# Optimization experiments

Hardware: AMD Instinct MI355X
Metric: run time of the kernel (lower is better)

## Reference

```python
import jax, jax.numpy as jnp
import numpy as np

N = 50000          # nodes
E = 1_600_000      # edges
H = 64             # agg_hidden (heads=1, concat)
IN = 7             # in_channels
EDIM = 4           # edge_dim
G = 256            # num graphs in batch
FC = 128           # fc_hidden
NC = 2             # num_classes
SLOPE = 0.2        # GATv2 LeakyReLU negative slope


def setup_inputs() -> dict:
    key = jax.random.key(0)
    ks = jax.random.split(key, 24)
    s = 0.1
    d = {
        "x": jax.random.normal(ks[0], (N, IN), dtype=jnp.float32),
        "edge_index": jax.random.randint(ks[1], (2, E), 0, N, dtype=jnp.int32),
        "edge_attr": jax.random.normal(ks[2], (E, EDIM), dtype=jnp.float32),
        "batch": jnp.sort(jax.random.randint(ks[3], (N,), 0, G, dtype=jnp.int32)),
        # GATv2 layer 0 (in=7 -> 64)
        "Wl0": jax.random.normal(ks[4], (IN, H)) * s,
        "bl0": jnp.zeros((H,), jnp.float32),
        "Wr0": jax.random.normal(ks[5], (IN, H)) * s,
        "br0": jnp.zeros((H,), jnp.float32),
        "We0": jax.random.normal(ks[6], (EDIM, H)) * s,
        "att0": jax.random.normal(ks[7], (H,)) * s,
        "bias0": jnp.zeros((H,), jnp.float32),
        # GATv2 layer 1 (64 -> 64)
        "Wl1": jax.random.normal(ks[8], (H, H)) * s,
        "bl1": jnp.zeros((H,), jnp.float32),
        "Wr1": jax.random.normal(ks[9], (H, H)) * s,
        "br1": jnp.zeros((H,), jnp.float32),
        "We1": jax.random.normal(ks[10], (EDIM, H)) * s,
        "att1": jax.random.normal(ks[11], (H,)) * s,
        "bias1": jnp.zeros((H,), jnp.float32),
        # MLP head
        "fc1_w": jax.random.normal(ks[12], (H, FC)) * s,
        "fc1_b": jnp.zeros((FC,), jnp.float32),
        "fc2_w": jax.random.normal(ks[13], (FC, NC)) * s,
        "fc2_b": jnp.zeros((NC,), jnp.float32),
    }
    return d


def _gatv2(x, src, dst, edge_attr, Wl, bl, Wr, br, We, att, bias):
    # GATv2Conv (heads=1, concat=True, edge_dim=EDIM), eval mode (no dropout)
    xl = x @ Wl + bl                         # source-side projection [N,H]
    xr = x @ Wr + br                         # target-side projection [N,H]
    e = xl[src] + xr[dst] + edge_attr @ We   # per-edge pre-activation [E,H]
    score = jax.nn.leaky_relu(e, SLOPE) @ att  # [E]
    # segment softmax over destination nodes
    m = jax.ops.segment_max(score, dst, num_segments=N)
    ex = jnp.exp(score - m[dst])
    den = jax.ops.segment_sum(ex, dst, num_segments=N)
    alpha = ex / (den[dst] + 1e-16)
    out = jax.ops.segment_sum(xl[src] * alpha[:, None], dst, num_segments=N)
    return out + bias


def reference(x, edge_index, edge_attr, batch,
              Wl0, bl0, Wr0, br0, We0, att0, bias0,
              Wl1, bl1, Wr1, br1, We1, att1, bias1,
              fc1_w, fc1_b, fc2_w, fc2_b):
    src, dst = edge_index[0], edge_index[1]
    h = jax.nn.elu(_gatv2(x, src, dst, edge_attr, Wl0, bl0, Wr0, br0, We0, att0, bias0))
    h = jax.nn.elu(_gatv2(h, src, dst, edge_attr, Wl1, bl1, Wr1, br1, We1, att1, bias1))
    # global mean pool over graphs
    sums = jax.ops.segment_sum(h, batch, num_segments=G)
    cnt = jax.ops.segment_sum(jnp.ones((h.shape[0],), h.dtype), batch, num_segments=G)
    g = sums / jnp.maximum(cnt, 1.0)[:, None]      # [G,H]
    g = jax.nn.relu(g @ fc1_w + fc1_b)
    logits = g @ fc2_w + fc2_b
    return jax.nn.log_softmax(logits, axis=1)
```

## Files before the change

### kernel.cpp

```cpp
#include <hip/hip_runtime.h>
#include <hip/hip_fp16.h>

#define N_NODES 50000
#define N_EDGES 1600000
#define H 64
#define IN_CH 7
#define EDIM 4
#define G_GRAPHS 256
#define FC 128
#define NC 2
#define SLOPE 0.2f
#define NBUCK 196
#define EPB1 8192
#define NB1 ((N_EDGES + EPB1 - 1) / EPB1)
#define PAIR_BLOCKS ((N_NODES * 32 + 255) / 256)

typedef _Float16 h2v __attribute__((ext_vector_type(2)));

__device__ __forceinline__ float fdot2f(h2v a, h2v b, float c) {
#if defined(__has_builtin) && __has_builtin(__builtin_amdgcn_fdot2)
    return __builtin_amdgcn_fdot2(a, b, c, false);
#else
    return c + (float)a[0] * (float)b[0] + (float)a[1] * (float)b[1];
#endif
}

__device__ __forceinline__ float wave_sum_to63(float x) {
    x += __int_as_float(__builtin_amdgcn_update_dpp(0, __float_as_int(x), 0x111, 0xf, 0xf, true));
    x += __int_as_float(__builtin_amdgcn_update_dpp(0, __float_as_int(x), 0x112, 0xf, 0xf, true));
    x += __int_as_float(__builtin_amdgcn_update_dpp(0, __float_as_int(x), 0x114, 0xf, 0xf, true));
    x += __int_as_float(__builtin_amdgcn_update_dpp(0, __float_as_int(x), 0x118, 0xf, 0xf, true));
    x += __int_as_float(__builtin_amdgcn_update_dpp(0, __float_as_int(x), 0x142, 0xf, 0xf, true));
    x += __int_as_float(__builtin_amdgcn_update_dpp(0, __float_as_int(x), 0x143, 0xf, 0xf, true));
    return x;
}
__device__ __forceinline__ float lane63_bcast(float x) {
    return __int_as_float(__builtin_amdgcn_readlane(__float_as_int(x), 63));
}
__device__ __forceinline__ float readlane_f(float x, int i) {
    return __int_as_float(__builtin_amdgcn_readlane(__float_as_int(x), i));
}

__device__ __forceinline__ float gat_score(int4 ent,
        const __half2* __restrict__ xlh, const __half2* __restrict__ xrh,
        const __half2* __restrict__ weh, const __half2* __restrict__ atth) {
    __half2 ea01 = *reinterpret_cast<__half2*>(&ent.y);
    __half2 ea23 = *reinterpret_cast<__half2*>(&ent.z);
    __half2 e0 = __half2half2(__low2half(ea01));
    __half2 e1 = __half2half2(__high2half(ea01));
    __half2 e2 = __half2half2(__low2half(ea23));
    __half2 e3 = __half2half2(__high2half(ea23));
    const h2v sl = { (_Float16)SLOPE, (_Float16)SLOPE };
    const int4* xa = (const int4*)(xlh + (size_t)ent.x * 32);
    const int4* xb = (const int4*)(xrh + (size_t)ent.w * 32);
    float acc0 = 0.f, acc1 = 0.f;
#pragma unroll
    for (int k = 0; k < 8; ++k) {
        int4 va = xa[k];
        int4 vb = xb[k];
        const __half2* ha = reinterpret_cast<const __half2*>(&va);
        const __half2* hc = reinterpret_cast<const __half2*>(&vb);
#pragma unroll
        for (int j = 0; j < 4; ++j) {
            int c = k * 4 + j;
            __half2 v2 = __hadd2(ha[j], hc[j]);
            v2 = __hfma2(e0, weh[c * 4 + 0], v2);
            v2 = __hfma2(e1, weh[c * 4 + 1], v2);
            v2 = __hfma2(e2, weh[c * 4 + 2], v2);
            v2 = __hfma2(e3, weh[c * 4 + 3], v2);
            h2v vv = *reinterpret_cast<h2v*>(&v2);
            h2v Lv = __builtin_elementwise_max(vv, sl * vv);
            __half2 av = atth[c];
            if (j & 1)
                acc1 = fdot2f(Lv, *reinterpret_cast<h2v*>(&av), acc1);
            else
                acc0 = fdot2f(Lv, *reinterpret_cast<h2v*>(&av), acc0);
        }
    }
    return acc0 + acc1;
}

__global__ __launch_bounds__(256) void front_kernel(
        const int* __restrict__ dst, int* __restrict__ rank1, int* __restrict__ bhist,
        const float* __restrict__ xin,
        const float* __restrict__ Wl0, const float* __restrict__ bl0,
        const float* __restrict__ Wr0, const float* __restrict__ br0,
        __half2* __restrict__ xlh, __half2* __restrict__ xrh,
        const float* __restrict__ We0, const float* __restrict__ We1,
        const float* __restrict__ Wl1, const float* __restrict__ bl1,
        const float* __restrict__ Wr1, const float* __restrict__ br1,
        __half2* __restrict__ weh0, __half2* __restrict__ weh1,
        __half2* __restrict__ wt, float* __restrict__ bb,
        const float* __restrict__ att0, const float* __restrict__ att1,
        __half2* __restrict__ atth0, __half2* __restrict__ atth1) {
    __shared__ int hist[NBUCK];
    int b = blockIdx.x;
    int t = threadIdx.x;
    if (b < NB1) {
        if (t < NBUCK) hist[t] = 0;
        __syncthreads();
#pragma unroll
        for (int i = 0; i < EPB1 / 256; ++i) {
            int e = b * EPB1 + i * 256 + t;
            if (e < N_EDGES) {
                int k = dst[e] >> 8;
                rank1[e] = atomicAdd(&hist[k], 1);
            }
        }
        __syncthreads();
        if (t < NBUCK) bhist[b * NBUCK + t] = hist[t];
    } else if (b < NB1 + PAIR_BLOCKS) {
        int idx = (b - NB1) * 256 + t;
        if (idx < N_NODES * 32) {
            int n = idx >> 5;
            int c = idx & 31;
            const float* xi = xin + n * IN_CH;
            float2 bl2 = ((const float2*)bl0)[c];
            float2 br2 = ((const float2*)br0)[c];
            float al0 = bl2.x, al1 = bl2.y, ar0 = br2.x, ar1 = br2.y;
#pragma unroll
            for (int k = 0; k < IN_CH; ++k) {
                float xv = xi[k];
                float2 wl2 = ((const float2*)(Wl0 + k * H))[c];
                float2 wr2 = ((const float2*)(Wr0 + k * H))[c];
                al0 += xv * wl2.x; al1 += xv * wl2.y;
                ar0 += xv * wr2.x; ar1 += xv * wr2.y;
            }
            xlh[idx] = __floats2half2_rn(al0, al1);
            xrh[idx] = __floats2half2_rn(ar0, ar1);
        }
    } else {
        if (t < 32) {
            for (int k = 0; k < 4; ++k)
                weh0[t * 4 + k] = __floats2half2_rn(We0[k * H + 2 * t], We0[k * H + 2 * t + 1]);
        } else if (t < 64) {
            int c = t - 32;
            for (int k = 0; k < 4; ++k)
                weh1[c * 4 + k] = __floats2half2_rn(We1[k * H + 2 * c], We1[k * H + 2 * c + 1]);
        }
        if (t < 128) {
            const float* W = (t < 64) ? Wl1 : Wr1;
            int c = t & 63;
            for (int kk = 0; kk < 32; ++kk)
                wt[t * 32 + kk] = __floats2half2_rn(W[(2 * kk) * H + c], W[(2 * kk + 1) * H + c]);
            bb[t] = (t < 64) ? bl1[c] : br1[c];
        } else if (t < 160) {
            int c = t - 128;
            atth0[c] = __floats2half2_rn(att0[2 * c], att0[2 * c + 1]);
            atth1[c] = __floats2half2_rn(att1[2 * c], att1[2 * c + 1]);
        }
    }
}

__global__ __launch_bounds__(256) void bucket_scan_kernel(
        const int* __restrict__ bhist, int* __restrict__ bases, int* __restrict__ cb_start) {
    __shared__ int lds[256];
    int t = threadIdx.x;
    int run = 0;
    if (t < NBUCK) {
        for (int b = 0; b < NB1; ++b) {
            bases[b * NBUCK + t] = run;
            run += bhist[b * NBUCK + t];
        }
    }
    lds[t] = (t < NBUCK) ? run : 0;
    __syncthreads();
    for (int off = 1; off < 256; off <<= 1) {
        int x = (t >= off) ? lds[t - off] : 0;
        __syncthreads();
        lds[t] += x;
        __syncthreads();
    }
    if (t < NBUCK) cb_start[t] = lds[t] - run;
    if (t == NBUCK - 1) cb_start[NBUCK] = lds[t];
}

__global__ void coarse_scatter_kernel(const int* __restrict__ src, const int* __restrict__ dst,
                                      const int* __restrict__ rank1, const int* __restrict__ bases,
                                      const int* __restrict__ cb_start,
                                      const float* __restrict__ edge_attr,
                                      int4* __restrict__ tmp) {
    int e = blockIdx.x * blockDim.x + threadIdx.x;
    if (e >= N_EDGES) return;
    int d = dst[e];
    int k = d >> 8;
    int b = e / EPB1;
    int slot = cb_start[k] + bases[b * NBUCK + k] + rank1[e];
    float4 ea = ((const float4*)edge_attr)[e];
    __half2 h01 = __floats2half2_rn(ea.x, ea.y);
    __half2 h23 = __floats2half2_rn(ea.z, ea.w);
    int4 ent;
    ent.x = src[e];
    ent.y = *reinterpret_cast<int*>(&h01);
    ent.z = *reinterpret_cast<int*>(&h23);
    ent.w = d;
    tmp[slot] = ent;
}

__global__ __launch_bounds__(1024) void fine_sort_kernel(
        const int* __restrict__ cb_start, const int4* __restrict__ tmp,
        const __half2* __restrict__ xlh, const __half2* __restrict__ xrh,
        const __half2* __restrict__ weh, const __half2* __restrict__ atth,
        int4* __restrict__ csr, int* __restrict__ srcs,
        int* __restrict__ row_start, float* __restrict__ escore) {
    __shared__ int hist2[256];
    __shared__ int cursor[256];
    __shared__ int lds[256];
    int k = blockIdx.x;
    int t = threadIdx.x;
    int beg = cb_start[k], end = cb_start[k + 1];
    if (t < 256) hist2[t] = 0;
    __syncthreads();
    for (int i = beg + t; i < end; i += 1024)
        atomicAdd(&hist2[tmp[i].w & 255], 1);
    __syncthreads();
    int v = (t < 256) ? hist2[t] : 0;
    if (t < 256) lds[t] = v;
    __syncthreads();
    for (int off = 1; off < 256; off <<= 1) {
        int x = 0;
        if (t < 256 && t >= off) x = lds[t - off];
        __syncthreads();
        if (t < 256) lds[t] += x;
        __syncthreads();
    }
    if (t < 256) {
        int pre = lds[t] - v;
        cursor[t] = pre;
        int node = k * 256 + t;
        if (node <= N_NODES) row_start[node] = beg + pre;
    }
    __syncthreads();
    for (int i = beg + t; i < end; i += 1024) {
        int4 ent = tmp[i];
        int slot = beg + atomicAdd(&cursor[ent.w & 255], 1);
        csr[slot] = ent;
        srcs[slot] = ent.x;
        escore[slot] = gat_score(ent, xlh, xrh, weh, atth);
    }
}

__global__ __launch_bounds__(256) void proj1_kernel(
        const float* __restrict__ xin,
        const __half2* __restrict__ wt,
        const float* __restrict__ bb,
        __half2* __restrict__ xlh, __half2* __restrict__ xrh) {
    int g = __builtin_amdgcn_readfirstlane((int)(threadIdx.x >> 6));
    int lane = threadIdx.x & 63;
    int node = blockIdx.x * 64 + lane;
    if (node >= N_NODES) return;

    h2v xrow[32];
    const float4* xp = (const float4*)(xin + node * 64);
#pragma unroll
    for (int q = 0; q < 16; ++q) {
        float4 v = xp[q];
        __half2 a = __floats2half2_rn(v.x, v.y);
        __half2 b = __floats2half2_rn(v.z, v.w);
        xrow[2 * q]     = *reinterpret_cast<h2v*>(&a);
        xrow[2 * q + 1] = *reinterpret_cast<h2v*>(&b);
    }

    __half2* outp = (g < 2) ? xlh : xrh;
    int chbase = g * 32;
    int localbase = (g & 1) * 16;

#pragma unroll
    for (int cp = 0; cp < 16; ++cp) {
        int ch0 = chbase + 2 * cp;
        const h2v* w0 = (const h2v*)(wt + ch0 * 32);
        const h2v* w1 = (const h2v*)(wt + (ch0 + 1) * 32);
        float a0 = bb[ch0], a1 = bb[ch0 + 1];
#pragma unroll
        for (int kk = 0; kk < 32; ++kk) {
            a0 = fdot2f(xrow[kk], w0[kk], a0);
            a1 = fdot2f(xrow[kk], w1[kk], a1);
        }
        outp[node * 32 + localbase + cp] = __floats2half2_rn(a0, a1);
    }
}

__global__ __launch_bounds__(256) void score_kernel(
        const int4* __restrict__ csr,
        const __half2* __restrict__ xlh, const __half2* __restrict__ xrh,
        const __half2* __restrict__ weh, const __half2* __restrict__ atth,
        float* __restrict__ score) {
    int e = blockIdx.x * 256 + threadIdx.x;
    score[e] = gat_score(csr[e], xlh, xrh, weh, atth);
}

__global__ __launch_bounds__(256) void agg_kernel(
        const int* __restrict__ row_start,
        const int* __restrict__ srcs,
        const float* __restrict__ score,
        const __half2* __restrict__ xlh,
        const float* __restrict__ bias,
        float* __restrict__ out) {
    int wave = (blockIdx.x * blockDim.x + threadIdx.x) >> 6;
    if (wave >= N_NODES) return;
    int lane = threadIdx.x & 63;
    int c = lane & 31;
    int hb = lane >> 5;
    int d = wave;
    int beg = __builtin_amdgcn_readfirstlane(row_start[d]);
    int end = __builtin_amdgcn_readfirstlane(row_start[d + 1]);

    float l_lane = 0.f;
    float ax0 = 0.f, ay0 = 0.f, ax1 = 0.f, ay1 = 0.f;

    for (int cbeg = beg; cbeg < end; cbeg += 64) {
        int n = end - cbeg;
        float sc = score[cbeg + lane];
        float p = __expf(sc);
        p = (lane < n) ? p : 0.f;
        l_lane += p;

        int nn = min(n, 64);
        int j = 0;
        for (; j + 4 <= nn; j += 4) {
            int sA0 = __builtin_amdgcn_readfirstlane(srcs[cbeg + j + 0]);
            int sB0 = __builtin_amdgcn_readfirstlane(srcs[cbeg + j + 1]);
            int sA1 = __builtin_amdgcn_readfirstlane(srcs[cbeg + j + 2]);
            int sB1 = __builtin_amdgcn_readfirstlane(srcs[cbeg + j + 3]);
            float pA0 = readlane_f(p, j + 0), pB0 = readlane_f(p, j + 1);
            float pA1 = readlane_f(p, j + 2), pB1 = readlane_f(p, j + 3);
            int s0 = hb ? sB0 : sA0;
            int s1 = hb ? sB1 : sA1;
            float pv0 = hb ? pB0 : pA0;
            float pv1 = hb ? pB1 : pA1;
            float2 x0 = __half22float2(xlh[s0 * 32 + c]);
            float2 x1 = __half22float2(xlh[s1 * 32 + c]);
            ax0 += pv0 * x0.x; ay0 += pv0 * x0.y;
            ax1 += pv1 * x1.x; ay1 += pv1 * x1.y;
        }
        for (; j + 2 <= nn; j += 2) {
            int sA = __builtin_amdgcn_readfirstlane(srcs[cbeg + j + 0]);
            int sB = __builtin_amdgcn_readfirstlane(srcs[cbeg + j + 1]);
            float pA = readlane_f(p, j + 0), pB = readlane_f(p, j + 1);
            int s = hb ? sB : sA;
            float pv = hb ? pB : pA;
            float2 xf = __half22float2(xlh[s * 32 + c]);
            ax0 += pv * xf.x; ay0 += pv * xf.y;
        }
        if (j < nn) {
            int sA = __builtin_amdgcn_readfirstlane(srcs[cbeg + j]);
            float pA = readlane_f(p, j);
            float pv = hb ? 0.f : pA;
            float2 xf = __half22float2(xlh[sA * 32 + c]);
            ax0 += pv * xf.x; ay0 += pv * xf.y;
        }
    }

    float l = lane63_bcast(wave_sum_to63(l_lane));
    float accx = ax0 + ax1, accy = ay0 + ay1;
    accx += __shfl_xor(accx, 32, 64);
    accy += __shfl_xor(accy, 32, 64);
    if (hb == 0) {
        float inv = 1.f / (l + 1e-16f);
        float2 b2 = ((const float2*)bias)[c];
        float o0 = accx * inv + b2.x;
        float o1 = accy * inv + b2.y;
        o0 = o0 > 0.f ? o0 : expm1f(o0);
        o1 = o1 > 0.f ? o1 : expm1f(o1);
        ((float2*)out)[d * 32 + c] = float2{o0, o1};
    }
}

__global__ __launch_bounds__(256) void pool_head_kernel(
        const float* __restrict__ h, const int* __restrict__ batch,
        const float* __restrict__ fc1w, const float* __restrict__ fc1b,
        const float* __restrict__ fc2w, const float* __restrict__ fc2b,
        float* __restrict__ out) {
    int g = blockIdx.x;
    int lo = 0, hi = N_NODES;
    while (lo < hi) { int mid = (lo + hi) >> 1; if (batch[mid] < g) lo = mid + 1; else hi = mid; }
    int start = lo;
    hi = N_NODES;
    while (lo < hi) { int mid = (lo + hi) >> 1; if (batch[mid] < g + 1) lo = mid + 1; else hi = mid; }
    int end = lo;

    int lane = threadIdx.x & 63;
    int w = threadIdx.x >> 6;
    float s = 0.f;
    for (int n = start + w; n < end; n += 4) s += h[n * H + lane];
    __shared__ float red[4][H];
    __shared__ float gv[H];
    __shared__ float f[FC];
    __shared__ float lg[NC];
    red[w][lane] = s;
    __syncthreads();
    if (w == 0) {
        float tot = red[0][lane] + red[1][lane] + red[2][lane] + red[3][lane];
        gv[lane] = tot / fmaxf((float)(end - start), 1.f);
    }
    __syncthreads();
    int t = threadIdx.x;
    if (t < FC) {
        float acc = fc1b[t];
#pragma unroll 16
        for (int k = 0; k < H; ++k) acc += gv[k] * fc1w[k * FC + t];
        f[t] = fmaxf(acc, 0.f);
    }
    __syncthreads();
    if (t < NC) {
        float a = fc2b[t];
        for (int k = 0; k < FC; ++k) a += f[k] * fc2w[k * NC + t];
        lg[t] = a;
    }
    __syncthreads();
    if (t < NC) {
        float mx = fmaxf(lg[0], lg[1]);
        float lse = mx + logf(expf(lg[0] - mx) + expf(lg[1] - mx));
        out[g * NC + t] = lg[t] - lse;
    }
}

extern "C" void kernel_launch(void* const* d_in, const int* in_sizes, int n_in,
                              void* d_out, int out_size, void* d_ws, size_t ws_size,
                              hipStream_t stream) {
    const float* x         = (const float*)d_in[0];
    const int*   edge_idx  = (const int*)d_in[1];
    const float* edge_attr = (const float*)d_in[2];
    const int*   batch     = (const int*)d_in[3];
    const float* Wl0  = (const float*)d_in[4];
    const float* bl0  = (const float*)d_in[5];
    const float* Wr0  = (const float*)d_in[6];
    const float* br0  = (const float*)d_in[7];
    const float* We0  = (const float*)d_in[8];
    const float* att0 = (const float*)d_in[9];
    const float* bias0= (const float*)d_in[10];
    const float* Wl1  = (const float*)d_in[11];
    const float* bl1  = (const float*)d_in[12];
    const float* Wr1  = (const float*)d_in[13];
    const float* br1  = (const float*)d_in[14];
    const float* We1  = (const float*)d_in[15];
    const float* att1 = (const float*)d_in[16];
    const float* bias1= (const float*)d_in[17];
    const float* fc1w = (const float*)d_in[18];
    const float* fc1b = (const float*)d_in[19];
    const float* fc2w = (const float*)d_in[20];
    const float* fc2b = (const float*)d_in[21];

    __half2* xlh    = (__half2*)d_ws;
    __half2* xrh    = xlh + N_NODES * 32;
    float* C        = (float*)(xrh + N_NODES * 32);
    int4*  tmp      = (int4*)C;
    int4*  csr      = (int4*)(tmp + N_EDGES);
    int*   srcs     = (int*)(csr + N_EDGES);
    int*   row_start= srcs + N_EDGES;
    int*   rank1    = row_start + N_NODES + 1;
    float* escore   = (float*)rank1;
    int*   bhist    = rank1 + N_EDGES;
    int*   bases    = bhist + NB1 * NBUCK;
    int*   cb_start = bases + NB1 * NBUCK;
    __half2* weh0   = (__half2*)(cb_start + NBUCK + 1);
    __half2* weh1   = weh0 + 128;
    __half2* wt1    = weh1 + 128;
    float* bb1      = (float*)(wt1 + 128 * 32);
    __half2* atth0  = (__half2*)(bb1 + 128);
    __half2* atth1  = atth0 + 32;

    const int* src = edge_idx;
    const int* dst = edge_idx + N_EDGES;

    const int edgeBlocks = (N_EDGES + 255) / 256;
    const int waveBlocks = (N_NODES * 64 + 255) / 256;
    const int p1Blocks   = (N_NODES + 63) / 64;
    const int frontBlocks = NB1 + PAIR_BLOCKS + 1;

    front_kernel<<<frontBlocks, 256, 0, stream>>>(dst, rank1, bhist,
                                                  x, Wl0, bl0, Wr0, br0, xlh, xrh,
                                                  We0, We1, Wl1, bl1, Wr1, br1,
                                                  weh0, weh1, wt1, bb1,
                                                  att0, att1, atth0, atth1);
    bucket_scan_kernel<<<1, 256, 0, stream>>>(bhist, bases, cb_start);
    coarse_scatter_kernel<<<edgeBlocks, 256, 0, stream>>>(src, dst, rank1, bases, cb_start,
                                                          edge_attr, tmp);
    fine_sort_kernel<<<NBUCK, 1024, 0, stream>>>(cb_start, tmp, xlh, xrh, weh0, atth0,
                                                 csr, srcs, row_start, escore);

    agg_kernel<<<waveBlocks, 256, 0, stream>>>(row_start, srcs, escore, xlh, bias0, C);

    proj1_kernel<<<p1Blocks, 256, 0, stream>>>(C, wt1, bb1, xlh, xrh);
    score_kernel<<<edgeBlocks, 256, 0, stream>>>(csr, xlh, xrh, weh1, atth1, escore);
    agg_kernel<<<waveBlocks, 256, 0, stream>>>(row_start, srcs, escore, xlh, bias1, C);

    pool_head_kernel<<<G_GRAPHS, 256, 0, stream>>>(C, batch, fc1w, fc1b, fc2w, fc2b, (float*)d_out);
}
```

Measured before the change: 444.6 us.

## Replace two-level bucket sort with global atomic counting sort into CSR

Replaces the coarse-bucket histogram, bucket scan, coarse scatter and per-bucket fine sort with a single pass of global atomics on per-node counts. A one-block node scan then builds row_start, and one scatter writes the CSR entries straight into their final slots. Layer-0 scores move out of the fine sort into a separate score_kernel launch. This drops the intermediate tmp buffer pass and the block-local sorting, but brings contended global atomics on 50k counters, a serial single-block scan, and nondeterministic edge order within each row.

```diff
diff --git a/kernel.cpp b/kernel.cpp
--- a/kernel.cpp
+++ b/kernel.cpp
@@ -10,7 +10,6 @@
 #define FC 128
 #define NC 2
 #define SLOPE 0.2f
-#define NBUCK 196
 #define EPB1 8192
 #define NB1 ((N_EDGES + EPB1 - 1) / EPB1)
 #define PAIR_BLOCKS ((N_NODES * 32 + 255) / 256)
@@ -81,7 +80,7 @@
 }
 
 __global__ __launch_bounds__(256) void front_kernel(
-        const int* __restrict__ dst, int* __restrict__ rank1, int* __restrict__ bhist,
+        const int* __restrict__ dst, int* __restrict__ rank1, int* __restrict__ cnt,
         const float* __restrict__ xin,
         const float* __restrict__ Wl0, const float* __restrict__ bl0,
         const float* __restrict__ Wr0, const float* __restrict__ br0,
@@ -93,22 +92,15 @@
         __half2* __restrict__ wt, float* __restrict__ bb,
         const float* __restrict__ att0, const float* __restrict__ att1,
         __half2* __restrict__ atth0, __half2* __restrict__ atth1) {
-    __shared__ int hist[NBUCK];
     int b = blockIdx.x;
     int t = threadIdx.x;
     if (b < NB1) {
-        if (t < NBUCK) hist[t] = 0;
-        __syncthreads();
 #pragma unroll
         for (int i = 0; i < EPB1 / 256; ++i) {
             int e = b * EPB1 + i * 256 + t;
-            if (e < N_EDGES) {
-                int k = dst[e] >> 8;
-                rank1[e] = atomicAdd(&hist[k], 1);
-            }
-        }
-        __syncthreads();
-        if (t < NBUCK) bhist[b * NBUCK + t] = hist[t];
+            if (e < N_EDGES)
+                rank1[e] = atomicAdd(&cnt[dst[e]], 1);
+        }
     } else if (b < NB1 + PAIR_BLOCKS) {
         int idx = (b - NB1) * 256 + t;
         if (idx < N_NODES * 32) {
@@ -152,40 +144,43 @@
     }
 }
 
-__global__ __launch_bounds__(256) void bucket_scan_kernel(
-        const int* __restrict__ bhist, int* __restrict__ bases, int* __restrict__ cb_start) {
-    __shared__ int lds[256];
-    int t = threadIdx.x;
-    int run = 0;
-    if (t < NBUCK) {
-        for (int b = 0; b < NB1; ++b) {
-            bases[b * NBUCK + t] = run;
-            run += bhist[b * NBUCK + t];
-        }
-    }
-    lds[t] = (t < NBUCK) ? run : 0;
-    __syncthreads();
-    for (int off = 1; off < 256; off <<= 1) {
-        int x = (t >= off) ? lds[t - off] : 0;
-        __syncthreads();
-        lds[t] += x;
-        __syncthreads();
-    }
-    if (t < NBUCK) cb_start[t] = lds[t] - run;
-    if (t == NBUCK - 1) cb_start[NBUCK] = lds[t];
-}
-
-__global__ void coarse_scatter_kernel(const int* __restrict__ src, const int* __restrict__ dst,
-                                      const int* __restrict__ rank1, const int* __restrict__ bases,
-                                      const int* __restrict__ cb_start,
-                                      const float* __restrict__ edge_attr,
-                                      int4* __restrict__ tmp) {
-    int e = blockIdx.x * blockDim.x + threadIdx.x;
-    if (e >= N_EDGES) return;
+__global__ __launch_bounds__(1024) void node_scan_kernel(
+        const int* __restrict__ cnt, int* __restrict__ row_start) {
+    __shared__ int wsum[16];
+    __shared__ int tot;
+    int t = threadIdx.x, lane = t & 63, w = t >> 6;
+    const int CHUNK = (N_NODES + 1023) / 1024;
+    int b0 = min(t * CHUNK, N_NODES);
+    int b1 = min(b0 + CHUNK, N_NODES);
+    int s = 0;
+    for (int i = b0; i < b1; ++i) s += cnt[i];
+    int sc = s;
+#pragma unroll
+    for (int off = 1; off < 64; off <<= 1) {
+        int x = __shfl_up(sc, off, 64);
+        if (lane >= off) sc += x;
+    }
+    if (lane == 63) wsum[w] = sc;
+    __syncthreads();
+    if (t == 0) {
+        int run = 0;
+        for (int j = 0; j < 16; ++j) { int v = wsum[j]; wsum[j] = run; run += v; }
+        tot = run;
+    }
+    __syncthreads();
+    int run = wsum[w] + sc - s;
+    for (int i = b0; i < b1; ++i) { int v = cnt[i]; row_start[i] = run; run += v; }
+    if (t == 0) row_start[N_NODES] = tot;
+}
+
+__global__ void scatter_kernel(const int* __restrict__ src, const int* __restrict__ dst,
+                               const int* __restrict__ rank1,
+                               const int* __restrict__ row_start,
+                               const float* __restrict__ edge_attr,
+                               int4* __restrict__ csr, int* __restrict__ srcs) {
+    int e = blockIdx.x * 256 + threadIdx.x;
     int d = dst[e];
-    int k = d >> 8;
-    int b = e / EPB1;
-    int slot = cb_start[k] + bases[b * NBUCK + k] + rank1[e];
+    int slot = row_start[d] + rank1[e];
     float4 ea = ((const float4*)edge_attr)[e];
     __half2 h01 = __floats2half2_rn(ea.x, ea.y);
     __half2 h23 = __floats2half2_rn(ea.z, ea.w);
@@ -194,50 +189,8 @@
     ent.y = *reinterpret_cast<int*>(&h01);
     ent.z = *reinterpret_cast<int*>(&h23);
     ent.w = d;
-    tmp[slot] = ent;
-}
-
-__global__ __launch_bounds__(1024) void fine_sort_kernel(
-        const int* __restrict__ cb_start, const int4* __restrict__ tmp,
-        const __half2* __restrict__ xlh, const __half2* __restrict__ xrh,
-        const __half2* __restrict__ weh, const __half2* __restrict__ atth,
-        int4* __restrict__ csr, int* __restrict__ srcs,
-        int* __restrict__ row_start, float* __restrict__ escore) {
-    __shared__ int hist2[256];
-    __shared__ int cursor[256];
-    __shared__ int lds[256];
-    int k = blockIdx.x;
-    int t = threadIdx.x;
-    int beg = cb_start[k], end = cb_start[k + 1];
-    if (t < 256) hist2[t] = 0;
-    __syncthreads();
-    for (int i = beg + t; i < end; i += 1024)
-        atomicAdd(&hist2[tmp[i].w & 255], 1);
-    __syncthreads();
-    int v = (t < 256) ? hist2[t] : 0;
-    if (t < 256) lds[t] = v;
-    __syncthreads();
-    for (int off = 1; off < 256; off <<= 1) {
-        int x = 0;
-        if (t < 256 && t >= off) x = lds[t - off];
-        __syncthreads();
-        if (t < 256) lds[t] += x;
-        __syncthreads();
-    }
-    if (t < 256) {
-        int pre = lds[t] - v;
-        cursor[t] = pre;
-        int node = k * 256 + t;
-        if (node <= N_NODES) row_start[node] = beg + pre;
-    }
-    __syncthreads();
-    for (int i = beg + t; i < end; i += 1024) {
-        int4 ent = tmp[i];
-        int slot = beg + atomicAdd(&cursor[ent.w & 255], 1);
-        csr[slot] = ent;
-        srcs[slot] = ent.x;
-        escore[slot] = gat_score(ent, xlh, xrh, weh, atth);
-    }
+    csr[slot] = ent;
+    srcs[slot] = ent.x;
 }
 
 __global__ __launch_bounds__(256) void proj1_kernel(
@@ -444,16 +397,14 @@
     __half2* xlh    = (__half2*)d_ws;
     __half2* xrh    = xlh + N_NODES * 32;
     float* C        = (float*)(xrh + N_NODES * 32);
-    int4*  tmp      = (int4*)C;
-    int4*  csr      = (int4*)(tmp + N_EDGES);
+    float* escore   = C + N_NODES * 64;
+    float* pad      = escore + N_EDGES;
+    int4*  csr      = (int4*)(pad + 64);
     int*   srcs     = (int*)(csr + N_EDGES);
     int*   row_start= srcs + N_EDGES;
     int*   rank1    = row_start + N_NODES + 1;
-    float* escore   = (float*)rank1;
-    int*   bhist    = rank1 + N_EDGES;
-    int*   bases    = bhist + NB1 * NBUCK;
-    int*   cb_start = bases + NB1 * NBUCK;
-    __half2* weh0   = (__half2*)(cb_start + NBUCK + 1);
+    int*   cnt      = rank1 + N_EDGES;
+    __half2* weh0   = (__half2*)(cnt + N_NODES);
     __half2* weh1   = weh0 + 128;
     __half2* wt1    = weh1 + 128;
     float* bb1      = (float*)(wt1 + 128 * 32);
@@ -468,17 +419,17 @@
     const int p1Blocks   = (N_NODES + 63) / 64;
     const int frontBlocks = NB1 + PAIR_BLOCKS + 1;
 
-    front_kernel<<<frontBlocks, 256, 0, stream>>>(dst, rank1, bhist,
+    hipMemsetAsync(cnt, 0, N_NODES * sizeof(int), stream);
+    front_kernel<<<frontBlocks, 256, 0, stream>>>(dst, rank1, cnt,
                                                   x, Wl0, bl0, Wr0, br0, xlh, xrh,
                                                   We0, We1, Wl1, bl1, Wr1, br1,
                                                   weh0, weh1, wt1, bb1,
                                                   att0, att1, atth0, atth1);
-    bucket_scan_kernel<<<1, 256, 0, stream>>>(bhist, bases, cb_start);
-    coarse_scatter_kernel<<<edgeBlocks, 256, 0, stream>>>(src, dst, rank1, bases, cb_start,
-                                                          edge_attr, tmp);
-    fine_sort_kernel<<<NBUCK, 1024, 0, stream>>>(cb_start, tmp, xlh, xrh, weh0, atth0,
-                                                 csr, srcs, row_start, escore);
-
+    node_scan_kernel<<<1, 1024, 0, stream>>>(cnt, row_start);
+    scatter_kernel<<<edgeBlocks, 256, 0, stream>>>(src, dst, rank1, row_start,
+                                                   edge_attr, csr, srcs);
+
+    score_kernel<<<edgeBlocks, 256, 0, stream>>>(csr, xlh, xrh, weh0, atth0, escore);
     agg_kernel<<<waveBlocks, 256, 0, stream>>>(row_start, srcs, escore, xlh, bias0, C);
 
     proj1_kernel<<<p1Blocks, 256, 0, stream>>>(C, wt1, bb1, xlh, xrh);
```

After: 515.4 us. +15.9%, slower.
